# Kernel optimization log

Measured on AMD Instinct MI355X. Metric: run time of the kernel, lower is better.

Reference implementation:

```python
import jax, jax.numpy as jnp
import numpy as np

N = 8192
IN_DIM = 512
OUT_DIM = 64
ALPHA = 0.2  # LeakyReLU negative slope
NEG_FILL = -9e15


def setup_inputs() -> dict:
    key = jax.random.key(0)
    k1, k2, k3, k4 = jax.random.split(key, 4)
    features = jax.random.normal(k1, (N, IN_DIM), dtype=jnp.float32)
    adj = jax.random.randint(k2, (N, N), 0, 2, dtype=jnp.int32)
    # xavier_normal with gain 1.414 ~ sqrt(2)
    W = jax.random.normal(k3, (IN_DIM, OUT_DIM), dtype=jnp.float32) * (1.414 * np.sqrt(2.0 / (IN_DIM + OUT_DIM)))
    a = jax.random.normal(k4, (2 * OUT_DIM, 1), dtype=jnp.float32) * (1.414 * np.sqrt(2.0 / (2 * OUT_DIM + 1)))
    return {"features": features, "adj": adj, "W": W, "a": a}


def reference(features, adj, W, a):
    h = features @ W                      # [N, OUT_DIM]
    h1 = h @ a[:OUT_DIM, :]               # [N, 1]
    h2 = h @ a[OUT_DIM:, :]               # [N, 1]
    e = h1 + h2.T                         # [N, N] broadcast add
    e = jnp.where(e > 0, e, ALPHA * e)    # LeakyReLU
    scores = jnp.where(adj > 0, e, NEG_FILL)
    attention = jax.nn.softmax(scores, axis=-1)
    out = attention @ h                   # [N, OUT_DIM]
    out = jax.nn.elu(out)                 # concat=True branch
    return out
```

## Files before the change

kernel.cpp:

```cpp
#include <hip/hip_runtime.h>
#include <hip/hip_bf16.h>

#define N 8192
#define IN_DIM 512
#define OUT_DIM 64
#define ALPHA 0.2f
#define LOG2E 1.44269504f

typedef __hip_bfloat16 bf16;
typedef __attribute__((ext_vector_type(8))) short bf16x8;
typedef __attribute__((ext_vector_type(4))) float f32x4;
typedef __attribute__((ext_vector_type(4))) int   int4v;
typedef __attribute__((ext_vector_type(4))) float float4v;

__device__ __forceinline__ float u2f(unsigned short u) {
    union { unsigned int i; float f; } c; c.i = ((unsigned int)u) << 16; return c.f;
}

__device__ __forceinline__ uint2 splitpack2(float f0, float f1) {
    unsigned u0 = __float_as_uint(f0), u1 = __float_as_uint(f1);
    unsigned h0 = u0 & 0xFFFF0000u, h1 = u1 & 0xFFFF0000u;
    float l0 = f0 - __uint_as_float(h0);
    float l1 = f1 - __uint_as_float(h1);
    uint2 r;
    r.x = (h0 >> 16) | h1;
    r.y = (__float_as_uint(l0) >> 16) | (__float_as_uint(l1) & 0xFFFF0000u);
    return r;
}

__device__ __forceinline__ bf16x8 as_bf16x8(int a, int b, int c, int d) {
    union { int4v i; bf16x8 b; } u;
    u.i = (int4v){a, b, c, d};
    return u.b;
}

__device__ __forceinline__ unsigned fenc(float f) {
    unsigned u = __float_as_uint(f);
    return (u & 0x80000000u) ? ~u : (u | 0x80000000u);
}
__device__ __forceinline__ float fdec(unsigned e) {
    return (e & 0x80000000u) ? __uint_as_float(e & 0x7FFFFFFFu) : __uint_as_float(~e);
}

__global__ void k_sniff(const unsigned short* __restrict__ feat_u16, int* __restrict__ flag) {
    int lane = threadIdx.x;
    float v = u2f(feat_u16[2 * lane]);
    float av = fabsf(v);
    int ok = (v == 0.f) || (av > 1e-8f && av < 1e8f);
    unsigned long long m = __ballot(ok);
    if (lane == 0) *flag = (__popcll(m) >= 48) ? 1 : 0;
}

__global__ __launch_bounds__(256) void k_prep(const void* __restrict__ Wv,
                                              const int* __restrict__ flag,
                                              unsigned short* __restrict__ WT_hi,
                                              unsigned short* __restrict__ WT_lo,
                                              unsigned* __restrict__ h2enc) {
    if (blockIdx.x == 0 && threadIdx.x == 0) *h2enc = fenc(-3e38f);
    int idx = blockIdx.x * 256 + threadIdx.x;
    int k = idx >> 6, c = idx & 63;
    float w = (*flag) ? u2f(((const unsigned short*)Wv)[idx]) : ((const float*)Wv)[idx];
    unsigned u = __float_as_uint(w);
    unsigned hi = u & 0xFFFF0000u;
    float lo = w - __uint_as_float(hi);
    WT_hi[c * IN_DIM + k] = (unsigned short)(hi >> 16);
    WT_lo[c * IN_DIM + k] = (unsigned short)(__float_as_uint(lo) >> 16);
}

__global__ __launch_bounds__(256) void k_h(const void* __restrict__ featv,
                                           const unsigned short* __restrict__ WT_hi,
                                           const unsigned short* __restrict__ WT_lo,
                                           const void* __restrict__ av,
                                           const int* __restrict__ flag,
                                           float* __restrict__ h1,
                                           float* __restrict__ h2,
                                           unsigned short* __restrict__ hT_hi,
                                           unsigned short* __restrict__ hT_lo,
                                           unsigned* __restrict__ h2enc) {
    __shared__ float C[16][66];
    const int tid = threadIdx.x;
    const int wave = tid >> 6;
    const int lane = tid & 63;
    const int rsub = lane & 15;
    const int g = lane >> 4;
    const int wrow0 = blockIdx.x * 16;
    const int isbf = *flag;

    f32x4 acc0 = {0.f,0.f,0.f,0.f}, acc1 = {0.f,0.f,0.f,0.f};
    f32x4 acc2 = {0.f,0.f,0.f,0.f}, acc3 = {0.f,0.f,0.f,0.f};

    const int kbeg = wave * (IN_DIM / 4);
    for (int k0 = kbeg; k0 < kbeg + IN_DIM / 4; k0 += 32) {
        const int ka = k0 + g * 8;
        bf16x8 Ah, Al;
        if (isbf) {
            Ah = *(const bf16x8*)((const unsigned short*)featv + (size_t)(wrow0 + rsub) * IN_DIM + ka);
            Al = as_bf16x8(0, 0, 0, 0);
        } else {
            const float* fp = (const float*)featv + (size_t)(wrow0 + rsub) * IN_DIM + ka;
            float4v f0 = *(const float4v*)fp;
            float4v f1 = *(const float4v*)(fp + 4);
            uint2 q0 = splitpack2(f0[0], f0[1]);
            uint2 q1 = splitpack2(f0[2], f0[3]);
            uint2 q2 = splitpack2(f1[0], f1[1]);
            uint2 q3 = splitpack2(f1[2], f1[3]);
            Ah = as_bf16x8((int)q0.x, (int)q1.x, (int)q2.x, (int)q3.x);
            Al = as_bf16x8((int)q0.y, (int)q1.y, (int)q2.y, (int)q3.y);
        }
        const unsigned short* wh = WT_hi + (size_t)rsub * IN_DIM + ka;
        const unsigned short* wl = WT_lo + (size_t)rsub * IN_DIM + ka;
        bf16x8 B0h = *(const bf16x8*)(wh);
        bf16x8 B1h = *(const bf16x8*)(wh + 16 * IN_DIM);
        bf16x8 B2h = *(const bf16x8*)(wh + 32 * IN_DIM);
        bf16x8 B3h = *(const bf16x8*)(wh + 48 * IN_DIM);
        bf16x8 B0l = *(const bf16x8*)(wl);
        bf16x8 B1l = *(const bf16x8*)(wl + 16 * IN_DIM);
        bf16x8 B2l = *(const bf16x8*)(wl + 32 * IN_DIM);
        bf16x8 B3l = *(const bf16x8*)(wl + 48 * IN_DIM);

        acc0 = __builtin_amdgcn_mfma_f32_16x16x32_bf16(Ah, B0h, acc0, 0, 0, 0);
        acc1 = __builtin_amdgcn_mfma_f32_16x16x32_bf16(Ah, B1h, acc1, 0, 0, 0);
        acc2 = __builtin_amdgcn_mfma_f32_16x16x32_bf16(Ah, B2h, acc2, 0, 0, 0);
        acc3 = __builtin_amdgcn_mfma_f32_16x16x32_bf16(Ah, B3h, acc3, 0, 0, 0);
        acc0 = __builtin_amdgcn_mfma_f32_16x16x32_bf16(Ah, B0l, acc0, 0, 0, 0);
        acc1 = __builtin_amdgcn_mfma_f32_16x16x32_bf16(Ah, B1l, acc1, 0, 0, 0);
        acc2 = __builtin_amdgcn_mfma_f32_16x16x32_bf16(Ah, B2l, acc2, 0, 0, 0);
        acc3 = __builtin_amdgcn_mfma_f32_16x16x32_bf16(Ah, B3l, acc3, 0, 0, 0);
        acc0 = __builtin_amdgcn_mfma_f32_16x16x32_bf16(Al, B0h, acc0, 0, 0, 0);
        acc1 = __builtin_amdgcn_mfma_f32_16x16x32_bf16(Al, B1h, acc1, 0, 0, 0);
        acc2 = __builtin_amdgcn_mfma_f32_16x16x32_bf16(Al, B2h, acc2, 0, 0, 0);
        acc3 = __builtin_amdgcn_mfma_f32_16x16x32_bf16(Al, B3h, acc3, 0, 0, 0);
    }

    if (wave == 0) {
#pragma unroll
        for (int r = 0; r < 4; ++r) {
            C[g * 4 + r][rsub]      = acc0[r];
            C[g * 4 + r][16 + rsub] = acc1[r];
            C[g * 4 + r][32 + rsub] = acc2[r];
            C[g * 4 + r][48 + rsub] = acc3[r];
        }
    }
    __syncthreads();
#pragma unroll
    for (int w2 = 1; w2 < 4; ++w2) {
        if (wave == w2) {
#pragma unroll
            for (int r = 0; r < 4; ++r) {
                C[g * 4 + r][rsub]      += acc0[r];
                C[g * 4 + r][16 + rsub] += acc1[r];
                C[g * 4 + r][32 + rsub] += acc2[r];
                C[g * 4 + r][48 + rsub] += acc3[r];
            }
        }
        __syncthreads();
    }

    {
        int c = tid >> 2;
        int r0 = (tid & 3) * 4;
        float v0 = C[r0 + 0][c], v1 = C[r0 + 1][c], v2 = C[r0 + 2][c], v3 = C[r0 + 3][c];
        uint2 s01 = splitpack2(v0, v1);
        uint2 s23 = splitpack2(v2, v3);
        size_t off = (size_t)c * N + wrow0 + r0;
        { uint2 ph; ph.x = s01.x; ph.y = s23.x; *(uint2*)(hT_hi + off) = ph; }
        { uint2 pl; pl.x = s01.y; pl.y = s23.y; *(uint2*)(hT_lo + off) = pl; }
    }

    if (wave == 0 && lane < 16) {
        const float* af = (const float*)av;
        const unsigned short* au = (const unsigned short*)av;
        float s1 = 0.f, s2 = 0.f;
#pragma unroll 8
        for (int c = 0; c < 64; ++c) {
            float a1 = isbf ? u2f(au[c])      : af[c];
            float a2 = isbf ? u2f(au[64 + c]) : af[64 + c];
            float hv = C[lane][c];
            s1 += hv * a1;
            s2 += hv * a2;
        }
        s1 *= LOG2E; s2 *= LOG2E;
        h1[wrow0 + lane] = s1;
        h2[wrow0 + lane] = s2;
        float wm = s2;
#pragma unroll
        for (int off = 8; off; off >>= 1) wm = fmaxf(wm, __shfl_xor(wm, off));
        if (lane == 0) atomicMax(h2enc, fenc(wm));
    }
}

__global__ __launch_bounds__(256, 2) void k_attn(const int* __restrict__ adj,
                                                 const float* __restrict__ h1,
                                                 const float* __restrict__ h2,
                                                 const unsigned short* __restrict__ hT_hi,
                                                 const unsigned short* __restrict__ hT_lo,
                                                 const unsigned* __restrict__ h2enc,
                                                 float* __restrict__ pacc,
                                                 float* __restrict__ plner,
                                                 int klen) {
    __shared__ float accs[64][66];
    __shared__ float lredL[4][64];

    const int wave = threadIdx.x >> 6;
    const int lane = threadIdx.x & 63;
    const int rsub = lane & 15;
    const int g = lane >> 4;
    const int row0 = blockIdx.x * 64;
    const int kbid = blockIdx.y;

    const float h2m = fdec(*h2enc);
    float h1r[4], c0[4];
#pragma unroll
    for (int mt = 0; mt < 4; ++mt) {
        h1r[mt] = h1[row0 + mt * 16 + rsub];
        float u = h1r[mt] + h2m;
        c0[mt] = -fmaxf(u, ALPHA * u);
    }

    f32x4 acc[4][4];
#pragma unroll
    for (int mt = 0; mt < 4; ++mt)
#pragma unroll
        for (int ct = 0; ct < 4; ++ct) acc[mt][ct] = (f32x4){0.f, 0.f, 0.f, 0.f};
    float lacc[4] = {0.f, 0.f, 0.f, 0.f};

    const unsigned short* bph = hT_hi + (size_t)rsub * N;
    const unsigned short* bpl = hT_lo + (size_t)rsub * N;

    const int kbeg = kbid * klen + wave * (klen >> 2);
    const int kend = kbeg + (klen >> 2);
    for (int k0 = kbeg; k0 < kend; k0 += 32) {
        const int kb = k0 + g * 8;

        const unsigned short* bh = bph + kb;
        const unsigned short* bl = bpl + kb;
        bf16x8 B0h = *(const bf16x8*)(bh);
        bf16x8 B1h = *(const bf16x8*)(bh + 16 * (size_t)N);
        bf16x8 B2h = *(const bf16x8*)(bh + 32 * (size_t)N);
        bf16x8 B3h = *(const bf16x8*)(bh + 48 * (size_t)N);
        bf16x8 B0l = *(const bf16x8*)(bl);
        bf16x8 B1l = *(const bf16x8*)(bl + 16 * (size_t)N);
        bf16x8 B2l = *(const bf16x8*)(bl + 32 * (size_t)N);
        bf16x8 B3l = *(const bf16x8*)(bl + 48 * (size_t)N);

        float4v hA = *(const float4v*)(h2 + kb);
        float4v hB = *(const float4v*)(h2 + kb + 4);

#pragma unroll
        for (int mt = 0; mt < 4; ++mt) {
            const size_t arow = (size_t)(row0 + mt * 16 + rsub) * N + kb;
            int4v aj0 = *(const int4v*)(adj + arow);
            int4v aj1 = *(const int4v*)(adj + arow + 4);

            float w[8];
#pragma unroll
            for (int j = 0; j < 4; ++j) {
                float u = h1r[mt] + hA[j];
                float s = fmaxf(u, ALPHA * u);
                float e = exp2f(s + c0[mt]);
                w[j] = aj0[j] > 0 ? e : 0.f;
            }
#pragma unroll
            for (int j = 0; j < 4; ++j) {
                float u = h1r[mt] + hB[j];
                float s = fmaxf(u, ALPHA * u);
                float e = exp2f(s + c0[mt]);
                w[4 + j] = aj1[j] > 0 ? e : 0.f;
            }
#pragma unroll
            for (int j = 0; j < 8; ++j) lacc[mt] += w[j];

            uint2 p0 = splitpack2(w[0], w[1]);
            uint2 p1 = splitpack2(w[2], w[3]);
            uint2 p2 = splitpack2(w[4], w[5]);
            uint2 p3 = splitpack2(w[6], w[7]);
            bf16x8 Ahi = as_bf16x8((int)p0.x, (int)p1.x, (int)p2.x, (int)p3.x);
            bf16x8 Alo = as_bf16x8((int)p0.y, (int)p1.y, (int)p2.y, (int)p3.y);

            acc[mt][0] = __builtin_amdgcn_mfma_f32_16x16x32_bf16(Ahi, B0h, acc[mt][0], 0, 0, 0);
            acc[mt][1] = __builtin_amdgcn_mfma_f32_16x16x32_bf16(Ahi, B1h, acc[mt][1], 0, 0, 0);
            acc[mt][2] = __builtin_amdgcn_mfma_f32_16x16x32_bf16(Ahi, B2h, acc[mt][2], 0, 0, 0);
            acc[mt][3] = __builtin_amdgcn_mfma_f32_16x16x32_bf16(Ahi, B3h, acc[mt][3], 0, 0, 0);
            acc[mt][0] = __builtin_amdgcn_mfma_f32_16x16x32_bf16(Ahi, B0l, acc[mt][0], 0, 0, 0);
            acc[mt][1] = __builtin_amdgcn_mfma_f32_16x16x32_bf16(Ahi, B1l, acc[mt][1], 0, 0, 0);
            acc[mt][2] = __builtin_amdgcn_mfma_f32_16x16x32_bf16(Ahi, B2l, acc[mt][2], 0, 0, 0);
            acc[mt][3] = __builtin_amdgcn_mfma_f32_16x16x32_bf16(Ahi, B3l, acc[mt][3], 0, 0, 0);
            acc[mt][0] = __builtin_amdgcn_mfma_f32_16x16x32_bf16(Alo, B0h, acc[mt][0], 0, 0, 0);
            acc[mt][1] = __builtin_amdgcn_mfma_f32_16x16x32_bf16(Alo, B1h, acc[mt][1], 0, 0, 0);
            acc[mt][2] = __builtin_amdgcn_mfma_f32_16x16x32_bf16(Alo, B2h, acc[mt][2], 0, 0, 0);
            acc[mt][3] = __builtin_amdgcn_mfma_f32_16x16x32_bf16(Alo, B3h, acc[mt][3], 0, 0, 0);
        }
    }

#pragma unroll
    for (int mt = 0; mt < 4; ++mt) {
        float l = lacc[mt];
        l += __shfl_xor(l, 16);
        l += __shfl_xor(l, 32);
        if (g == 0) lredL[wave][mt * 16 + rsub] = l;
    }

    if (wave == 0) {
#pragma unroll
        for (int mt = 0; mt < 4; ++mt)
#pragma unroll
            for (int ct = 0; ct < 4; ++ct)
#pragma unroll
                for (int r = 0; r < 4; ++r)
                    accs[mt * 16 + g * 4 + r][ct * 16 + rsub] = acc[mt][ct][r];
    }
    __syncthreads();
#pragma unroll
    for (int w2 = 1; w2 < 4; ++w2) {
        if (wave == w2) {
#pragma unroll
            for (int mt = 0; mt < 4; ++mt)
#pragma unroll
                for (int ct = 0; ct < 4; ++ct)
#pragma unroll
                    for (int r = 0; r < 4; ++r)
                        accs[mt * 16 + g * 4 + r][ct * 16 + rsub] += acc[mt][ct][r];
        }
        __syncthreads();
    }

    float* pa = pacc + (size_t)kbid * (N * OUT_DIM);
#pragma unroll
    for (int p = 0; p < 16; ++p) {
        int idx = p * 256 + threadIdx.x;
        int rl = idx >> 6, col = idx & 63;
        pa[(size_t)(row0 + rl) * OUT_DIM + col] = accs[rl][col];
    }
    if (threadIdx.x < 64)
        plner[(size_t)kbid * N + row0 + threadIdx.x] =
            lredL[0][threadIdx.x] + lredL[1][threadIdx.x] + lredL[2][threadIdx.x] + lredL[3][threadIdx.x];
}

__global__ __launch_bounds__(256) void k_out(const float* __restrict__ pacc,
                                             const float* __restrict__ plner,
                                             const int* __restrict__ flag,
                                             void* __restrict__ outv,
                                             int nkb) {
    int idx = blockIdx.x * 256 + threadIdx.x;
    int row = idx >> 6;
    float v = 0.f, l = 0.f;
    for (int kb = 0; kb < nkb; ++kb) {
        v += pacc[(size_t)kb * (N * OUT_DIM) + idx];
        l += plner[(size_t)kb * N + row];
    }
    float o = l > 0.f ? v / l : 0.f;
    o = o > 0.f ? o : exp2f(o * LOG2E) - 1.f;
    if (*flag) ((bf16*)outv)[idx] = __float2bfloat16(o);
    else       ((float*)outv)[idx] = o;
}

extern "C" void kernel_launch(void* const* d_in, const int* in_sizes, int n_in,
                              void* d_out, int out_size, void* d_ws, size_t ws_size,
                              hipStream_t stream) {
    const void* feat = d_in[0];
    const int* adj = (const int*)d_in[1];
    const void* W = d_in[2];
    const void* a = d_in[3];

    char* ws = (char*)d_ws;
    int*      flag  = (int*)(ws);
    unsigned* h2enc = (unsigned*)(ws + 256);
    float* h1       = (float*)(ws + 4096);
    float* h2       = (float*)(ws + 36864);
    unsigned short* hT_hi = (unsigned short*)(ws + 69632);
    unsigned short* hT_lo = (unsigned short*)(ws + 69632 + 1048576);
    unsigned short* WT_hi = (unsigned short*)(ws + 2166784);
    unsigned short* WT_lo = (unsigned short*)(ws + 2166784 + 65536);
    char* dynbase = ws + 2297856;

    size_t cap = ws_size ? ws_size : ((size_t)1 << 30);
    int nkb = 8;
    while (nkb > 1) {
        size_t need = 2297856 + (size_t)nkb * ((size_t)N * OUT_DIM * 4 + (size_t)N * 4);
        if (need <= cap) break;
        nkb >>= 1;
    }
    float* pacc  = (float*)dynbase;
    float* plner = (float*)(dynbase + (size_t)nkb * N * OUT_DIM * 4);

    hipLaunchKernelGGL(k_sniff, dim3(1), dim3(64), 0, stream,
                       (const unsigned short*)feat, flag);
    hipLaunchKernelGGL(k_prep, dim3((IN_DIM * OUT_DIM) / 256), dim3(256), 0, stream,
                       W, flag, WT_hi, WT_lo, h2enc);
    hipLaunchKernelGGL(k_h, dim3(N / 16), dim3(256), 0, stream,
                       feat, WT_hi, WT_lo, a, flag, h1, h2, hT_hi, hT_lo, h2enc);
    hipLaunchKernelGGL(k_attn, dim3(N / 64, nkb), dim3(256), 0, stream,
                       adj, h1, h2, hT_hi, hT_lo, h2enc, pacc, plner, N / nkb);
    hipLaunchKernelGGL(k_out, dim3((N * OUT_DIM) / 256), dim3(256), 0, stream,
                       pacc, plner, flag, d_out, nkb);
}
```

Baseline: 417.9 us.

## Permute hT columns for coalesced adj loads, use nontemporal adj reads, fuse sniff

Writes hT_hi/hT_lo with a permuted column order so that in the attention loop each lane group reads adj and h2 in two 16-byte chunks spaced 16 apart instead of one contiguous 32-byte run. This lets the four lane groups cover contiguous 64-byte spans per half, which should coalesce better. The adj reads now use nontemporal loads to avoid polluting cache with the streamed 256MB matrix. The dtype sniff kernel is folded into k_prep to save a launch, at the cost of every block redoing the sniff.

```diff
diff --git a/kernel.cpp b/kernel.cpp
--- a/kernel.cpp
+++ b/kernel.cpp
@@ -42,24 +42,31 @@
     return (e & 0x80000000u) ? __uint_as_float(e & 0x7FFFFFFFu) : __uint_as_float(~e);
 }
 
-__global__ void k_sniff(const unsigned short* __restrict__ feat_u16, int* __restrict__ flag) {
-    int lane = threadIdx.x;
-    float v = u2f(feat_u16[2 * lane]);
-    float av = fabsf(v);
-    int ok = (v == 0.f) || (av > 1e-8f && av < 1e8f);
-    unsigned long long m = __ballot(ok);
-    if (lane == 0) *flag = (__popcll(m) >= 48) ? 1 : 0;
-}
-
-__global__ __launch_bounds__(256) void k_prep(const void* __restrict__ Wv,
-                                              const int* __restrict__ flag,
+__device__ __forceinline__ int4v ntload4(const int* p) {
+    return __builtin_nontemporal_load((const int4v*)p);
+}
+
+__global__ __launch_bounds__(256) void k_prep(const unsigned short* __restrict__ feat_u16,
+                                              const void* __restrict__ Wv,
+                                              int* __restrict__ flag,
                                               unsigned short* __restrict__ WT_hi,
                                               unsigned short* __restrict__ WT_lo,
                                               unsigned* __restrict__ h2enc) {
-    if (blockIdx.x == 0 && threadIdx.x == 0) *h2enc = fenc(-3e38f);
-    int idx = blockIdx.x * 256 + threadIdx.x;
+    __shared__ int sflag;
+    int tid = threadIdx.x;
+    if (tid < 64) {
+        float v = u2f(feat_u16[2 * tid]);
+        float av = fabsf(v);
+        int ok = (v == 0.f) || (av > 1e-8f && av < 1e8f);
+        unsigned long long m = __ballot(ok);
+        if (tid == 0) sflag = (__popcll(m) >= 48) ? 1 : 0;
+    }
+    __syncthreads();
+    int isbf = sflag;
+    if (blockIdx.x == 0 && tid == 0) { *flag = isbf; *h2enc = fenc(-3e38f); }
+    int idx = blockIdx.x * 256 + tid;
     int k = idx >> 6, c = idx & 63;
-    float w = (*flag) ? u2f(((const unsigned short*)Wv)[idx]) : ((const float*)Wv)[idx];
+    float w = isbf ? u2f(((const unsigned short*)Wv)[idx]) : ((const float*)Wv)[idx];
     unsigned u = __float_as_uint(w);
     unsigned hi = u & 0xFFFF0000u;
     float lo = w - __uint_as_float(hi);
@@ -159,10 +166,12 @@
     {
         int c = tid >> 2;
         int r0 = (tid & 3) * 4;
+        int a = wrow0 + r0;
+        int dest = (a & ~31) + 8 * ((a >> 2) & 3) + 4 * ((a >> 4) & 1);
         float v0 = C[r0 + 0][c], v1 = C[r0 + 1][c], v2 = C[r0 + 2][c], v3 = C[r0 + 3][c];
         uint2 s01 = splitpack2(v0, v1);
         uint2 s23 = splitpack2(v2, v3);
-        size_t off = (size_t)c * N + wrow0 + r0;
+        size_t off = (size_t)c * N + dest;
         { uint2 ph; ph.x = s01.x; ph.y = s23.x; *(uint2*)(hT_hi + off) = ph; }
         { uint2 pl; pl.x = s01.y; pl.y = s23.y; *(uint2*)(hT_lo + off) = pl; }
     }
@@ -231,6 +240,8 @@
     const int kend = kbeg + (klen >> 2);
     for (int k0 = kbeg; k0 < kend; k0 += 32) {
         const int kb = k0 + g * 8;
+        const int ca = k0 + g * 4;
+        const int cb = k0 + 16 + g * 4;
 
         const unsigned short* bh = bph + kb;
         const unsigned short* bl = bpl + kb;
@@ -243,14 +254,14 @@
         bf16x8 B2l = *(const bf16x8*)(bl + 32 * (size_t)N);
         bf16x8 B3l = *(const bf16x8*)(bl + 48 * (size_t)N);
 
-        float4v hA = *(const float4v*)(h2 + kb);
-        float4v hB = *(const float4v*)(h2 + kb + 4);
+        float4v hA = *(const float4v*)(h2 + ca);
+        float4v hB = *(const float4v*)(h2 + cb);
 
 #pragma unroll
         for (int mt = 0; mt < 4; ++mt) {
-            const size_t arow = (size_t)(row0 + mt * 16 + rsub) * N + kb;
-            int4v aj0 = *(const int4v*)(adj + arow);
-            int4v aj1 = *(const int4v*)(adj + arow + 4);
+            const size_t arow = (size_t)(row0 + mt * 16 + rsub) * N;
+            int4v aj0 = ntload4(adj + arow + ca);
+            int4v aj1 = ntload4(adj + arow + cb);
 
             float w[8];
 #pragma unroll
@@ -383,10 +394,8 @@
     float* pacc  = (float*)dynbase;
     float* plner = (float*)(dynbase + (size_t)nkb * N * OUT_DIM * 4);
 
-    hipLaunchKernelGGL(k_sniff, dim3(1), dim3(64), 0, stream,
-                       (const unsigned short*)feat, flag);
     hipLaunchKernelGGL(k_prep, dim3((IN_DIM * OUT_DIM) / 256), dim3(256), 0, stream,
-                       W, flag, WT_hi, WT_lo, h2enc);
+                       (const unsigned short*)feat, W, flag, WT_hi, WT_lo, h2enc);
     hipLaunchKernelGGL(k_h, dim3(N / 16), dim3(256), 0, stream,
                        feat, WT_hi, WT_lo, a, flag, h1, h2, hT_hi, hT_lo, h2enc);
     hipLaunchKernelGGL(k_attn, dim3(N / 64, nkb), dim3(256), 0, stream,
```

Measured after the change: 436.0 us. 4.3% more time.
